# Optimization experiments

Measured on AMD Instinct MI355X. Metric: run time of the kernel, lower is better.

The kernel has to match this reference:

```python
import jax, jax.numpy as jnp
import numpy as np

H = 1280          # hidden_size
R = 8             # number of OFT blocks
BS = H // R       # block_size = 160
HEADS = 20
HD = H // HEADS   # head_dim = 64
CONSTRAINT = 0.001 * H  # = 1.28, as in __init__
EPS = 1e-8


def _cayley_blocks(W, constraint):
    # W: [r, bs, bs] -> per-block orthogonal rotation via Cayley transform
    Q = W - jnp.swapaxes(W, 1, 2)                       # skew-symmetric blocks
    n = jnp.linalg.norm(Q)                              # norm over ALL blocks flattened
    Q = Q * ((jnp.minimum(n, constraint) + EPS) / (n + EPS))
    I = jnp.eye(Q.shape[-1], dtype=Q.dtype)
    return jnp.matmul(I + Q, jnp.linalg.inv(I - Q))     # [r, bs, bs]


def _block_rotate(x, Rb):
    # x @ block_diag(Rb) done as a batched small matmul (no dense HxH matrix)
    B, S, _ = x.shape
    r, bs, _ = Rb.shape
    return jnp.einsum('bsrc,rcd->bsrd', x.reshape(B, S, r, bs), Rb).reshape(B, S, r * bs)


def setup_inputs() -> dict:
    key = jax.random.key(0)
    ks = jax.random.split(key, 10)
    B, S, Se, C = 16, 1024, 77, 768
    return {
        'hidden_states': jax.random.normal(ks[0], (B, S, H), jnp.float32),
        'encoder_hidden_states': jax.random.normal(ks[1], (B, Se, C), jnp.float32),
        'W_Q': jax.random.normal(ks[2], (R, BS, BS), jnp.float32) * 0.02,
        'W_K': jax.random.normal(ks[3], (R, BS, BS), jnp.float32) * 0.02,
        'W_V': jax.random.normal(ks[4], (R, BS, BS), jnp.float32) * 0.02,
        'Wq': jax.random.normal(ks[5], (H, H), jnp.float32) * (1.0 / np.float32(np.sqrt(H))),
        'Wk': jax.random.normal(ks[6], (C, H), jnp.float32) * (1.0 / np.float32(np.sqrt(C))),
        'Wv': jax.random.normal(ks[7], (C, H), jnp.float32) * (1.0 / np.float32(np.sqrt(C))),
        'Wo': jax.random.normal(ks[8], (H, H), jnp.float32) * (1.0 / np.float32(np.sqrt(H))),
        'bo': jnp.zeros((H,), jnp.float32),
    }


def reference(hidden_states, encoder_hidden_states, W_Q, W_K, W_V, Wq, Wk, Wv, Wo, bo):
    # linear projections (diffusers to_q/to_k/to_v, no bias)
    q = hidden_states @ Wq                      # [B, S, H]
    k = encoder_hidden_states @ Wk              # [B, Se, H]
    v = encoder_hidden_states @ Wv              # [B, Se, H]

    # OFT block-diagonal orthogonal rotations
    q = _block_rotate(q, _cayley_blocks(W_Q, CONSTRAINT))
    k = _block_rotate(k, _cayley_blocks(W_K, CONSTRAINT))
    v = _block_rotate(v, _cayley_blocks(W_V, CONSTRAINT))

    B, S, _ = q.shape
    Se = k.shape[1]
    qh = q.reshape(B, S, HEADS, HD)
    kh = k.reshape(B, Se, HEADS, HD)
    vh = v.reshape(B, Se, HEADS, HD)

    scale = np.float32(1.0 / np.sqrt(HD))
    scores = jnp.einsum('bqhd,bkhd->bhqk', qh, kh) * scale   # [B, heads, S, Se]
    probs = jax.nn.softmax(scores, axis=-1)
    out = jnp.einsum('bhqk,bkhd->bqhd', probs, vh).reshape(B, S, H)

    # to_out[0] linear (+bias); to_out[1] dropout is identity at eval
    return out @ Wo + bo
```

## Files before the change

### kernel.cpp

```cpp
#include <hip/hip_runtime.h>
#include <cstddef>
#include <cstdint>

#define H 1280
#define RB 8
#define BS 160
#define HEADS 20
#define HD 64
#define BATCH 16
#define SEQ 1024
#define SE 77
#define CENC 768
#define CONSTR 1.28f
#define EPS_N 1e-8f

#define QS_OFF    0u
#define PA_OFF    614400u
#define PB_OFF    1228800u
#define WQF_OFF   1843200u
#define WKF_OFF   3481600u
#define WVF_OFF   4464640u
#define QBUF_OFF  5447680u
#define KBUF_OFF  26419200u
#define VBUF_OFF  27996160u
#define HIDH_OFF  29573120u
#define HIDL_OFF  40058880u
#define ENCH_OFF  50544640u
#define ENCL_OFF  51017728u
#define WQTH_OFF  51490816u
#define WQTL_OFF  52310016u
#define WKTH_OFF  53129216u
#define WKTL_OFF  53620736u
#define WVTH_OFF  54112256u
#define WVTL_OFF  54603776u
#define WOTH_OFF  55095296u
#define WOTL_OFF  55914496u

typedef __attribute__((ext_vector_type(8))) short short8v;
typedef __attribute__((ext_vector_type(4))) float f32x4;

__device__ __forceinline__ short f2bf(float x) {
  unsigned u = __float_as_uint(x);
  unsigned r = (u + 0x7fffu + ((u >> 16) & 1u)) >> 16;
  return (short)r;
}
__device__ __forceinline__ float bf2f(short h) {
  return __uint_as_float(((unsigned)(unsigned short)h) << 16);
}

__global__ __launch_bounds__(1024) void skew_kernel(
    const float* __restrict__ W0, const float* __restrict__ W1,
    const float* __restrict__ W2, float* __restrict__ Qs) {
  int w = blockIdx.x;
  const float* W = (w == 0) ? W0 : ((w == 1) ? W1 : W2);
  float* Qout = Qs + (size_t)w * RB * BS * BS;
  __shared__ float red[1024];
  __shared__ float s_scale;
  float local = 0.f;
  for (int idx = threadIdx.x; idx < RB * BS * BS; idx += 1024) {
    int r = idx / (BS * BS);
    int rem = idx % (BS * BS);
    int i = rem / BS, j = rem % BS;
    float q = W[idx] - W[r * BS * BS + j * BS + i];
    local += q * q;
  }
  red[threadIdx.x] = local;
  __syncthreads();
  for (int s = 512; s > 0; s >>= 1) {
    if (threadIdx.x < (unsigned)s) red[threadIdx.x] += red[threadIdx.x + s];
    __syncthreads();
  }
  if (threadIdx.x == 0) {
    float n = sqrtf(red[0]);
    s_scale = (fminf(n, CONSTR) + EPS_N) / (n + EPS_N);
  }
  __syncthreads();
  float sc = s_scale;
  for (int idx = threadIdx.x; idx < RB * BS * BS; idx += 1024) {
    int r = idx / (BS * BS);
    int rem = idx % (BS * BS);
    int i = rem / BS, j = rem % BS;
    Qout[idx] = (W[idx] - W[r * BS * BS + j * BS + i]) * sc;
  }
}

__global__ __launch_bounds__(256) void horner_kernel(
    const float* __restrict__ Qs, const float* __restrict__ Pin,
    float* __restrict__ Pout) {
  int wr = blockIdx.x / 25;
  int st = blockIdx.x % 25;
  int is = st / 5, js = st % 5;
  const float* Ag = Qs + (size_t)wr * BS * BS;
  const float* Bg = Pin + (size_t)wr * BS * BS;
  float* Og = Pout + (size_t)wr * BS * BS;
  __shared__ float As[32 * 160];
  __shared__ float Bsh[160 * 32];
  for (int idx = threadIdx.x; idx < 32 * 160; idx += 256) {
    int rr = idx / 160, c = idx % 160;
    As[idx] = Ag[(is * 32 + rr) * 160 + c];
    int k = idx / 32, jj = idx % 32;
    int jglob = js * 32 + jj;
    float v = Bg[k * 160 + jglob];
    if (k == jglob) v += 1.f;
    Bsh[k * 32 + jj] = v;
  }
  __syncthreads();
  int ti = threadIdx.x / 32, tj = threadIdx.x % 32;
  float a0 = 0.f, a1 = 0.f, a2 = 0.f, a3 = 0.f;
  for (int k = 0; k < 160; ++k) {
    float b = Bsh[k * 32 + tj];
    a0 += As[(ti)*160 + k] * b;
    a1 += As[(ti + 8) * 160 + k] * b;
    a2 += As[(ti + 16) * 160 + k] * b;
    a3 += As[(ti + 24) * 160 + k] * b;
  }
  Og[(is * 32 + ti) * 160 + js * 32 + tj] = a0;
  Og[(is * 32 + ti + 8) * 160 + js * 32 + tj] = a1;
  Og[(is * 32 + ti + 16) * 160 + js * 32 + tj] = a2;
  Og[(is * 32 + ti + 24) * 160 + js * 32 + tj] = a3;
}

__global__ __launch_bounds__(256) void fold_kernel(
    const float* __restrict__ Wq, const float* __restrict__ Wk,
    const float* __restrict__ Wv, const float* __restrict__ P,
    float* __restrict__ WqF, float* __restrict__ WkF,
    float* __restrict__ WvF) {
  int r = blockIdx.x;
  int rt = blockIdx.y;
  int w = blockIdx.z;
  int rows = (w == 0) ? H : CENC;
  if (rt * 64 >= rows) return;
  const float* Wg = (w == 0) ? Wq : ((w == 1) ? Wk : Wv);
  float* Og = (w == 0) ? WqF : ((w == 1) ? WkF : WvF);
  const float* Pg = P + (size_t)(w * RB + r) * BS * BS;
  __shared__ float As[64 * 160];
  __shared__ float Ps[160 * 32];
  for (int idx = threadIdx.x; idx < 64 * 160; idx += 256) {
    int rr = idx / 160, c = idx % 160;
    As[idx] = Wg[(size_t)(rt * 64 + rr) * H + r * 160 + c];
  }
  int ti = threadIdx.x / 32, tc = threadIdx.x % 32;
  for (int strip = 0; strip < 5; ++strip) {
    __syncthreads();
    for (int idx = threadIdx.x; idx < 160 * 32; idx += 256) {
      int d = idx / 32, cc = idx % 32;
      Ps[idx] = Pg[d * 160 + strip * 32 + cc];
    }
    __syncthreads();
    float acc[8];
#pragma unroll
    for (int m = 0; m < 8; m++) acc[m] = 0.f;
    for (int d = 0; d < 160; ++d) {
      float p = Ps[d * 32 + tc];
#pragma unroll
      for (int m = 0; m < 8; m++) acc[m] += As[(ti * 8 + m) * 160 + d] * p;
    }
#pragma unroll
    for (int m = 0; m < 8; m++) {
      int row = ti * 8 + m;
      Og[(size_t)(rt * 64 + row) * H + r * 160 + strip * 32 + tc] =
          As[row * 160 + strip * 32 + tc] + 2.f * acc[m];
    }
  }
}

__global__ __launch_bounds__(256) void split_kernel(
    const float* __restrict__ in, short* __restrict__ hi,
    short* __restrict__ lo, int n4) {
  int stride = gridDim.x * 256;
  for (int idx = blockIdx.x * 256 + threadIdx.x; idx < n4; idx += stride) {
    float4 v = ((const float4*)in)[idx];
    short h0 = f2bf(v.x), h1 = f2bf(v.y), h2 = f2bf(v.z), h3 = f2bf(v.w);
    short l0 = f2bf(v.x - bf2f(h0));
    short l1 = f2bf(v.y - bf2f(h1));
    short l2 = f2bf(v.z - bf2f(h2));
    short l3 = f2bf(v.w - bf2f(h3));
    ((short4*)hi)[idx] = make_short4(h0, h1, h2, h3);
    ((short4*)lo)[idx] = make_short4(l0, l1, l2, l3);
  }
}

__global__ __launch_bounds__(256) void tsplit_kernel(
    const float* __restrict__ in, short* __restrict__ hi,
    short* __restrict__ lo, int Kdim, int Ndim) {
  __shared__ float tile[32][33];
  int kb = blockIdx.x * 32, nb = blockIdx.y * 32;
  int tx = threadIdx.x & 31, ty = threadIdx.x >> 5;
  for (int r = ty; r < 32; r += 8)
    tile[r][tx] = in[(size_t)(kb + r) * Ndim + nb + tx];
  __syncthreads();
  for (int r = ty; r < 32; r += 8) {
    float x = tile[tx][r];
    short h = f2bf(x);
    short l = f2bf(x - bf2f(h));
    size_t o = (size_t)(nb + r) * Kdim + kb + tx;
    hi[o] = h;
    lo[o] = l;
  }
}

__global__ __launch_bounds__(256, 2) void gemm_mfma(
    const short* __restrict__ Ah, const short* __restrict__ Al,
    const short* __restrict__ Bh, const short* __restrict__ Bl,
    float* __restrict__ C, int M, int N, int K,
    const float* __restrict__ bias) {
  __shared__ __align__(16) short As[2][128][40];
  __shared__ __align__(16) short Bs[2][128][40];
  int t = threadIdx.x;
  int m0 = blockIdx.x * 128, n0 = blockIdx.y * 128;
  int wv = t >> 6, l = t & 63;
  int wm = (wv >> 1) * 64, wn = (wv & 1) * 64;
  f32x4 acc[4][4];
#pragma unroll
  for (int m = 0; m < 4; m++)
#pragma unroll
    for (int n = 0; n < 4; n++) acc[m][n] = (f32x4){0.f, 0.f, 0.f, 0.f};

  int lr = l & 15;
  int kq = (l >> 4) * 8;

  for (int k0 = 0; k0 < K; k0 += 32) {
    __syncthreads();
#pragma unroll
    for (int i = 0; i < 2; ++i) {
      int idx = t + i * 256;
      int row = idx >> 2, c = idx & 3;
      int ar = m0 + row;
      if (ar >= M) ar = M - 1;
      size_t ga = (size_t)ar * K + k0 + c * 8;
      size_t gb = (size_t)(n0 + row) * K + k0 + c * 8;
      *(short8v*)&As[0][row][c * 8] = *(const short8v*)&Ah[ga];
      *(short8v*)&As[1][row][c * 8] = *(const short8v*)&Al[ga];
      *(short8v*)&Bs[0][row][c * 8] = *(const short8v*)&Bh[gb];
      *(short8v*)&Bs[1][row][c * 8] = *(const short8v*)&Bl[gb];
    }
    __syncthreads();
    short8v ah[4], al[4], bh[4], bl[4];
#pragma unroll
    for (int m = 0; m < 4; ++m) {
      ah[m] = *(const short8v*)&As[0][wm + m * 16 + lr][kq];
      al[m] = *(const short8v*)&As[1][wm + m * 16 + lr][kq];
    }
#pragma unroll
    for (int n = 0; n < 4; ++n) {
      bh[n] = *(const short8v*)&Bs[0][wn + n * 16 + lr][kq];
      bl[n] = *(const short8v*)&Bs[1][wn + n * 16 + lr][kq];
    }
#pragma unroll
    for (int m = 0; m < 4; ++m)
#pragma unroll
      for (int n = 0; n < 4; ++n) {
        acc[m][n] = __builtin_amdgcn_mfma_f32_16x16x32_bf16(ah[m], bh[n],
                                                            acc[m][n], 0, 0, 0);
        acc[m][n] = __builtin_amdgcn_mfma_f32_16x16x32_bf16(ah[m], bl[n],
                                                            acc[m][n], 0, 0, 0);
        acc[m][n] = __builtin_amdgcn_mfma_f32_16x16x32_bf16(al[m], bh[n],
                                                            acc[m][n], 0, 0, 0);
      }
  }

  int rbase = m0 + wm + (l >> 4) * 4;
#pragma unroll
  for (int n = 0; n < 4; ++n) {
    int col = n0 + wn + n * 16 + lr;
    float bv = bias ? bias[col] : 0.f;
#pragma unroll
    for (int m = 0; m < 4; ++m) {
#pragma unroll
      for (int r = 0; r < 4; ++r) {
        int row = rbase + m * 16 + r;
        if (row < M) C[(size_t)row * N + col] = acc[m][n][r] + bv;
      }
    }
  }
}

__global__ __launch_bounds__(256) void attn_kernel(
    const float* __restrict__ qbuf, const float* __restrict__ kbuf,
    const float* __restrict__ vbuf, short* __restrict__ aoh,
    short* __restrict__ aol) {
  int bid = blockIdx.x;
  int qt = bid % 16;
  int h = (bid / 16) % HEADS;
  int b = bid / (16 * HEADS);
  int s0 = qt * 64;
  __shared__ float Ks[SE * 64];
  __shared__ float Vs[SE * 64];
  __shared__ float Ss[SE * 64];
  int t = threadIdx.x;
  for (int idx = t; idx < SE * 64; idx += 256) {
    int j = idx / 64, d = idx % 64;
    Ks[idx] = kbuf[(size_t)(b * SE + j) * H + h * 64 + d];
    Vs[idx] = vbuf[(size_t)(b * SE + j) * H + h * 64 + d];
  }
  __syncthreads();
  int qi = t % 64;
  int grp = t / 64;
  const float* qrow = qbuf + (size_t)(b * SEQ + s0 + qi) * H + h * 64;
  float4 qr[16];
#pragma unroll
  for (int dd = 0; dd < 16; ++dd) qr[dd] = *(const float4*)&qrow[dd * 4];
  for (int j = grp; j < SE; j += 4) {
    float acc = 0.f;
#pragma unroll
    for (int dd = 0; dd < 16; ++dd) {
      float4 k4 = *(const float4*)&Ks[j * 64 + dd * 4];
      acc += qr[dd].x * k4.x + qr[dd].y * k4.y + qr[dd].z * k4.z +
             qr[dd].w * k4.w;
    }
    Ss[j * 64 + qi] = acc * 0.125f;
  }
  __syncthreads();
  if (t < 64) {
    float m = -1e30f;
    for (int j = 0; j < SE; ++j) m = fmaxf(m, Ss[j * 64 + t]);
    float sum = 0.f;
    for (int j = 0; j < SE; ++j) {
      float e = __expf(Ss[j * 64 + t] - m);
      Ss[j * 64 + t] = e;
      sum += e;
    }
    float inv = 1.f / sum;
    for (int j = 0; j < SE; ++j) Ss[j * 64 + t] *= inv;
  }
  __syncthreads();
  int d = t % 64;
  int qg = t / 64;
  float acc[16];
#pragma unroll
  for (int m = 0; m < 16; m++) acc[m] = 0.f;
  for (int j = 0; j < SE; ++j) {
    float v = Vs[j * 64 + d];
#pragma unroll
    for (int m = 0; m < 16; m++) acc[m] += Ss[j * 64 + qg * 16 + m] * v;
  }
#pragma unroll
  for (int m = 0; m < 16; m++) {
    size_t o = (size_t)(b * SEQ + s0 + qg * 16 + m) * H + h * 64 + d;
    float v = acc[m];
    short hh = f2bf(v);
    aoh[o] = hh;
    aol[o] = f2bf(v - bf2f(hh));
  }
}

extern "C" void kernel_launch(void* const* d_in, const int* in_sizes, int n_in,
                              void* d_out, int out_size, void* d_ws,
                              size_t ws_size, hipStream_t stream) {
  const float* hidden = (const float*)d_in[0];
  const float* enc = (const float*)d_in[1];
  const float* W_Q = (const float*)d_in[2];
  const float* W_K = (const float*)d_in[3];
  const float* W_V = (const float*)d_in[4];
  const float* Wq = (const float*)d_in[5];
  const float* Wk = (const float*)d_in[6];
  const float* Wv = (const float*)d_in[7];
  const float* Wo = (const float*)d_in[8];
  const float* bo = (const float*)d_in[9];
  float* out = (float*)d_out;
  float* ws = (float*)d_ws;

  float* Qs = ws + QS_OFF;
  float* Pa = ws + PA_OFF;
  float* Pb = ws + PB_OFF;
  float* WqF = ws + WQF_OFF;
  float* WkF = ws + WKF_OFF;
  float* WvF = ws + WVF_OFF;
  float* qbuf = ws + QBUF_OFF;
  float* kbuf = ws + KBUF_OFF;
  float* vbuf = ws + VBUF_OFF;
  short* HidH = (short*)(ws + HIDH_OFF);
  short* HidL = (short*)(ws + HIDL_OFF);
  short* EncH = (short*)(ws + ENCH_OFF);
  short* EncL = (short*)(ws + ENCL_OFF);
  short* WqTh = (short*)(ws + WQTH_OFF);
  short* WqTl = (short*)(ws + WQTL_OFF);
  short* WkTh = (short*)(ws + WKTH_OFF);
  short* WkTl = (short*)(ws + WKTL_OFF);
  short* WvTh = (short*)(ws + WVTH_OFF);
  short* WvTl = (short*)(ws + WVTL_OFF);
  short* WoTh = (short*)(ws + WOTH_OFF);
  short* WoTl = (short*)(ws + WOTL_OFF);
  short* AOh = HidH;
  short* AOl = HidL;

  skew_kernel<<<3, 1024, 0, stream>>>(W_Q, W_K, W_V, Qs);
  horner_kernel<<<600, 256, 0, stream>>>(Qs, Qs, Pa);
  horner_kernel<<<600, 256, 0, stream>>>(Qs, Pa, Pb);
  horner_kernel<<<600, 256, 0, stream>>>(Qs, Pb, Pa);
  horner_kernel<<<600, 256, 0, stream>>>(Qs, Pa, Pb);
  horner_kernel<<<600, 256, 0, stream>>>(Qs, Pb, Pa);
  fold_kernel<<<dim3(8, 20, 3), 256, 0, stream>>>(Wq, Wk, Wv, Pa, WqF, WkF,
                                                  WvF);

  tsplit_kernel<<<dim3(40, 40), 256, 0, stream>>>(WqF, WqTh, WqTl, H, H);
  tsplit_kernel<<<dim3(24, 40), 256, 0, stream>>>(WkF, WkTh, WkTl, CENC, H);
  tsplit_kernel<<<dim3(24, 40), 256, 0, stream>>>(WvF, WvTh, WvTl, CENC, H);
  tsplit_kernel<<<dim3(40, 40), 256, 0, stream>>>(Wo, WoTh, WoTl, H, H);

  split_kernel<<<2048, 256, 0, stream>>>(hidden, HidH, HidL,
                                         (BATCH * SEQ * H) / 4);
  split_kernel<<<512, 256, 0, stream>>>(enc, EncH, EncL,
                                        (BATCH * SE * CENC) / 4);

  gemm_mfma<<<dim3(128, 10), 256, 0, stream>>>(HidH, HidL, WqTh, WqTl, qbuf,
                                               BATCH * SEQ, H, H, nullptr);
  gemm_mfma<<<dim3(10, 10), 256, 0, stream>>>(EncH, EncL, WkTh, WkTl, kbuf,
                                              BATCH * SE, H, CENC, nullptr);
  gemm_mfma<<<dim3(10, 10), 256, 0, stream>>>(EncH, EncL, WvTh, WvTl, vbuf,
                                              BATCH * SE, H, CENC, nullptr);

  attn_kernel<<<BATCH * HEADS * (SEQ / 64), 256, 0, stream>>>(qbuf, kbuf, vbuf,
                                                              AOh, AOl);

  gemm_mfma<<<dim3(128, 10), 256, 0, stream>>>(AOh, AOl, WoTh, WoTl, out,
                                               BATCH * SEQ, H, H, bo);
}
```

Before: 1.237 ms.

## Parallelize skew-norm across blocks and restructure attention to reuse K/V tiles

The single-block-per-weight skew/norm kernel becomes a per-block partial norm with atomic accumulation, followed by a fully parallel scale kernel. This removes a serial 3-block launch. The attention kernel now processes 256 query rows per block in four sub-tiles, so each K/V load is reused four times. It spreads the QK dot products over 4 lanes per query with shuffle reductions instead of a single-thread softmax, and pads the shared-memory layouts to avoid bank conflicts. The cost is fewer blocks (1280 vs 5120), extra syncs per sub-tile, and atomics whose accumulation order is nondeterministic.

After: 4.112 ms. +232.6%, slower.

```diff
diff --git a/kernel.cpp b/kernel.cpp
--- a/kernel.cpp
+++ b/kernel.cpp
@@ -48,40 +48,47 @@
   return __uint_as_float(((unsigned)(unsigned short)h) << 16);
 }
 
-__global__ __launch_bounds__(1024) void skew_kernel(
+__global__ void zero_norms(float* __restrict__ norms) {
+  if (threadIdx.x < 3) norms[threadIdx.x] = 0.f;
+}
+
+__global__ __launch_bounds__(256) void skew_norm_kernel(
     const float* __restrict__ W0, const float* __restrict__ W1,
-    const float* __restrict__ W2, float* __restrict__ Qs) {
-  int w = blockIdx.x;
-  const float* W = (w == 0) ? W0 : ((w == 1) ? W1 : W2);
-  float* Qout = Qs + (size_t)w * RB * BS * BS;
-  __shared__ float red[1024];
-  __shared__ float s_scale;
+    const float* __restrict__ W2, float* __restrict__ norms) {
+  int wr = blockIdx.x;
+  int w = wr >> 3, r = wr & 7;
+  const float* Wb =
+      ((w == 0) ? W0 : ((w == 1) ? W1 : W2)) + (size_t)r * BS * BS;
   float local = 0.f;
-  for (int idx = threadIdx.x; idx < RB * BS * BS; idx += 1024) {
-    int r = idx / (BS * BS);
-    int rem = idx % (BS * BS);
-    int i = rem / BS, j = rem % BS;
-    float q = W[idx] - W[r * BS * BS + j * BS + i];
+  for (int idx = threadIdx.x; idx < BS * BS; idx += 256) {
+    int i = idx / BS, j = idx % BS;
+    float q = Wb[idx] - Wb[j * BS + i];
     local += q * q;
   }
-  red[threadIdx.x] = local;
+#pragma unroll
+  for (int off = 32; off > 0; off >>= 1) local += __shfl_down(local, off);
+  __shared__ float wsum[4];
+  if ((threadIdx.x & 63) == 0) wsum[threadIdx.x >> 6] = local;
   __syncthreads();
-  for (int s = 512; s > 0; s >>= 1) {
-    if (threadIdx.x < (unsigned)s) red[threadIdx.x] += red[threadIdx.x + s];
-    __syncthreads();
-  }
-  if (threadIdx.x == 0) {
-    float n = sqrtf(red[0]);
-    s_scale = (fminf(n, CONSTR) + EPS_N) / (n + EPS_N);
-  }
-  __syncthreads();
-  float sc = s_scale;
-  for (int idx = threadIdx.x; idx < RB * BS * BS; idx += 1024) {
-    int r = idx / (BS * BS);
-    int rem = idx % (BS * BS);
-    int i = rem / BS, j = rem % BS;
-    Qout[idx] = (W[idx] - W[r * BS * BS + j * BS + i]) * sc;
-  }
+  if (threadIdx.x == 0)
+    atomicAdd(&norms[w], wsum[0] + wsum[1] + wsum[2] + wsum[3]);
+}
+
+__global__ __launch_bounds__(256) void skew_scale_kernel(
+    const float* __restrict__ W0, const float* __restrict__ W1,
+    const float* __restrict__ W2, const float* __restrict__ norms,
+    float* __restrict__ Qs) {
+  int idx = blockIdx.x * 256 + threadIdx.x;
+  int w = idx / (RB * BS * BS);
+  int rem = idx - w * (RB * BS * BS);
+  int r = rem / (BS * BS);
+  int ij = rem - r * (BS * BS);
+  int i = ij / BS, j = ij - i * BS;
+  const float* Wb =
+      ((w == 0) ? W0 : ((w == 1) ? W1 : W2)) + (size_t)r * BS * BS;
+  float n = sqrtf(norms[w]);
+  float sc = (fminf(n, CONSTR) + EPS_N) / (n + EPS_N);
+  Qs[idx] = (Wb[ij] - Wb[j * BS + i]) * sc;
 }
 
 __global__ __launch_bounds__(256) void horner_kernel(
@@ -280,67 +287,100 @@
     const float* __restrict__ vbuf, short* __restrict__ aoh,
     short* __restrict__ aol) {
   int bid = blockIdx.x;
-  int qt = bid % 16;
-  int h = (bid / 16) % HEADS;
-  int b = bid / (16 * HEADS);
-  int s0 = qt * 64;
-  __shared__ float Ks[SE * 64];
-  __shared__ float Vs[SE * 64];
-  __shared__ float Ss[SE * 64];
+  int qb = bid & 3;
+  int h = (bid >> 2) % HEADS;
+  int b = bid / (4 * HEADS);
+  __shared__ float Ks[SE * 68];
+  __shared__ float Vs[80 * 64];
+  __shared__ float Ps[64 * 84];
   int t = threadIdx.x;
-  for (int idx = t; idx < SE * 64; idx += 256) {
-    int j = idx / 64, d = idx % 64;
-    Ks[idx] = kbuf[(size_t)(b * SE + j) * H + h * 64 + d];
-    Vs[idx] = vbuf[(size_t)(b * SE + j) * H + h * 64 + d];
-  }
+  for (int idx = t; idx < 80 * 64; idx += 256) {
+    int j = idx >> 6, d = idx & 63;
+    float kv = 0.f, vv = 0.f;
+    if (j < SE) {
+      size_t g = (size_t)(b * SE + j) * H + h * 64 + d;
+      kv = kbuf[g];
+      vv = vbuf[g];
+      Ks[j * 68 + d] = kv;
+    }
+    Vs[idx] = vv;
+  }
+  for (int idx = t; idx < 64 * 84; idx += 256) Ps[idx] = 0.f;
   __syncthreads();
-  int qi = t % 64;
-  int grp = t / 64;
-  const float* qrow = qbuf + (size_t)(b * SEQ + s0 + qi) * H + h * 64;
-  float4 qr[16];
-#pragma unroll
-  for (int dd = 0; dd < 16; ++dd) qr[dd] = *(const float4*)&qrow[dd * 4];
-  for (int j = grp; j < SE; j += 4) {
-    float acc = 0.f;
-#pragma unroll
-    for (int dd = 0; dd < 16; ++dd) {
-      float4 k4 = *(const float4*)&Ks[j * 64 + dd * 4];
-      acc += qr[dd].x * k4.x + qr[dd].y * k4.y + qr[dd].z * k4.z +
-             qr[dd].w * k4.w;
-    }
-    Ss[j * 64 + qi] = acc * 0.125f;
-  }
-  __syncthreads();
-  if (t < 64) {
+
+  int qi = t >> 2, sl = t & 3;
+  int dPV = t & 63, qg = t >> 6;
+
+  for (int sub = 0; sub < 4; ++sub) {
+    int qrow0 = b * SEQ + qb * 256 + sub * 64;
+    const float* qp = qbuf + (size_t)(qrow0 + qi) * H + h * 64;
+    float4 qr[16];
+#pragma unroll
+    for (int dd = 0; dd < 16; ++dd) qr[dd] = *(const float4*)&qp[dd * 4];
+
+    float s[20];
     float m = -1e30f;
-    for (int j = 0; j < SE; ++j) m = fmaxf(m, Ss[j * 64 + t]);
+#pragma unroll
+    for (int k = 0; k < 20; ++k) {
+      int j = sl + 4 * k;
+      float acc = -1e30f;
+      if (j < SE) {
+        acc = 0.f;
+#pragma unroll
+        for (int dd = 0; dd < 16; ++dd) {
+          float4 k4 = *(const float4*)&Ks[j * 68 + dd * 4];
+          acc += qr[dd].x * k4.x + qr[dd].y * k4.y + qr[dd].z * k4.z +
+                 qr[dd].w * k4.w;
+        }
+        acc *= 0.125f;
+      }
+      s[k] = acc;
+      m = fmaxf(m, acc);
+    }
+    m = fmaxf(m, __shfl_xor(m, 1));
+    m = fmaxf(m, __shfl_xor(m, 2));
     float sum = 0.f;
-    for (int j = 0; j < SE; ++j) {
-      float e = __expf(Ss[j * 64 + t] - m);
-      Ss[j * 64 + t] = e;
-      sum += e;
-    }
+#pragma unroll
+    for (int k = 0; k < 20; ++k) {
+      int j = sl + 4 * k;
+      if (j < SE) {
+        s[k] = __expf(s[k] - m);
+        sum += s[k];
+      }
+    }
+    sum += __shfl_xor(sum, 1);
+    sum += __shfl_xor(sum, 2);
     float inv = 1.f / sum;
-    for (int j = 0; j < SE; ++j) Ss[j * 64 + t] *= inv;
-  }
-  __syncthreads();
-  int d = t % 64;
-  int qg = t / 64;
-  float acc[16];
-#pragma unroll
-  for (int m = 0; m < 16; m++) acc[m] = 0.f;
-  for (int j = 0; j < SE; ++j) {
-    float v = Vs[j * 64 + d];
-#pragma unroll
-    for (int m = 0; m < 16; m++) acc[m] += Ss[j * 64 + qg * 16 + m] * v;
-  }
-#pragma unroll
-  for (int m = 0; m < 16; m++) {
-    size_t o = (size_t)(b * SEQ + s0 + qg * 16 + m) * H + h * 64 + d;
-    float v = acc[m];
-    short hh = f2bf(v);
-    aoh[o] = hh;
-    aol[o] = f2bf(v - bf2f(hh));
+#pragma unroll
+    for (int k = 0; k < 20; ++k) {
+      int j = sl + 4 * k;
+      if (j < SE) Ps[qi * 84 + j] = s[k] * inv;
+    }
+    __syncthreads();
+
+    float acc[16];
+#pragma unroll
+    for (int mm = 0; mm < 16; mm++) acc[mm] = 0.f;
+    for (int j4 = 0; j4 < 80; j4 += 4) {
+      float v0 = Vs[(j4 + 0) * 64 + dPV];
+      float v1 = Vs[(j4 + 1) * 64 + dPV];
+      float v2 = Vs[(j4 + 2) * 64 + dPV];
+      float v3 = Vs[(j4 + 3) * 64 + dPV];
+#pragma unroll
+      for (int mm = 0; mm < 16; mm++) {
+        float4 p4 = *(const float4*)&Ps[(qg * 16 + mm) * 84 + j4];
+        acc[mm] += p4.x * v0 + p4.y * v1 + p4.z * v2 + p4.w * v3;
+      }
+    }
+#pragma unroll
+    for (int mm = 0; mm < 16; mm++) {
+      size_t o = (size_t)(qrow0 + qg * 16 + mm) * H + h * 64 + dPV;
+      float v = acc[mm];
+      short hh = f2bf(v);
+      aoh[o] = hh;
+      aol[o] = f2bf(v - bf2f(hh));
+    }
+    __syncthreads();
   }
 }
 
@@ -383,8 +423,11 @@
   short* WoTl = (short*)(ws + WOTL_OFF);
   short* AOh = HidH;
   short* AOl = HidL;
-
-  skew_kernel<<<3, 1024, 0, stream>>>(W_Q, W_K, W_V, Qs);
+  float* norms = Pa;
+
+  zero_norms<<<1, 64, 0, stream>>>(norms);
+  skew_norm_kernel<<<24, 256, 0, stream>>>(W_Q, W_K, W_V, norms);
+  skew_scale_kernel<<<2400, 256, 0, stream>>>(W_Q, W_K, W_V, norms, Qs);
   horner_kernel<<<600, 256, 0, stream>>>(Qs, Qs, Pa);
   horner_kernel<<<600, 256, 0, stream>>>(Qs, Pa, Pb);
   horner_kernel<<<600, 256, 0, stream>>>(Qs, Pb, Pa);
@@ -410,8 +453,8 @@
   gemm_mfma<<<dim3(10, 10), 256, 0, stream>>>(EncH, EncL, WvTh, WvTl, vbuf,
                                               BATCH * SE, H, CENC, nullptr);
 
-  attn_kernel<<<BATCH * HEADS * (SEQ / 64), 256, 0, stream>>>(qbuf, kbuf, vbuf,
-                                                              AOh, AOl);
+  attn_kernel<<<BATCH * HEADS * 4, 256, 0, stream>>>(qbuf, kbuf, vbuf, AOh,
+                                                     AOl);
 
   gemm_mfma<<<dim3(128, 10), 256, 0, stream>>>(AOh, AOl, WoTh, WoTl, out,
                                                BATCH * SEQ, H, H, bo);
```
